# Kernel tuning notes

Hardware: AMD Instinct MI355X
Metric: run time of the kernel (lower is better)

## Reference

```python
import jax, jax.numpy as jnp
import numpy as np

D_MODEL, D_STATE, D_CONV, D_INNER, DT_RANK, K = 96, 16, 3, 192, 6, 4
B, H, W = 1, 64, 64


def setup_inputs() -> dict:
    key = jax.random.key(0)
    ks = jax.random.split(key, 10)
    x = jax.random.normal(ks[0], (B, H, W, D_MODEL), jnp.float32)
    in_proj_w = jax.random.normal(ks[1], (2 * D_INNER, D_MODEL), jnp.float32) * 0.02
    conv_w = jax.random.normal(ks[2], (D_INNER, 1, D_CONV, D_CONV), jnp.float32) * 0.1
    conv_b = jnp.zeros((D_INNER,), jnp.float32)
    x_proj_w = jax.random.normal(ks[3], (K, DT_RANK + 2 * D_STATE, D_INNER), jnp.float32) * 0.02
    dt_std = DT_RANK ** -0.5
    dt_w = jax.random.uniform(ks[4], (K, D_INNER, DT_RANK), jnp.float32, -dt_std, dt_std)
    # dt bias init: inv-softplus of dt ~ logUniform(1e-3, 1e-1)
    u = jax.random.uniform(ks[5], (K, D_INNER), jnp.float32)
    dt = jnp.exp(u * (np.log(0.1) - np.log(0.001)) + np.log(0.001)).clip(1e-4)
    dt_b = dt + jnp.log(-jnp.expm1(-dt))
    A_logs = jnp.log(jnp.broadcast_to(jnp.arange(1, D_STATE + 1, dtype=jnp.float32), (K * D_INNER, D_STATE)))
    Ds = jnp.ones((K * D_INNER,), jnp.float32)
    ln_g = jnp.ones((D_INNER,), jnp.float32)
    ln_b = jnp.zeros((D_INNER,), jnp.float32)
    out_proj_w = jax.random.normal(ks[6], (D_MODEL, D_INNER), jnp.float32) * 0.02
    return dict(x=x, in_proj_w=in_proj_w, conv_w=conv_w, conv_b=conv_b, x_proj_w=x_proj_w,
                dt_w=dt_w, dt_b=dt_b, A_logs=A_logs, Ds=Ds, ln_g=ln_g, ln_b=ln_b,
                out_proj_w=out_proj_w)


def _ss2d(x, in_proj_w, conv_w, conv_b, x_proj_w, dt_w, dt_b, A_logs, Ds, ln_g, ln_b, out_proj_w):
    b, h, w, c = x.shape
    L = h * w
    d = conv_w.shape[0]            # d_inner
    n = A_logs.shape[1]            # d_state
    r = dt_w.shape[2]              # dt_rank
    # in_proj + split
    xz = jnp.einsum('bhwc,ec->bhwe', x, in_proj_w)
    xx, z = xz[..., :d], xz[..., d:]
    # depthwise conv (NCHW) + SiLU
    xc = xx.transpose(0, 3, 1, 2)
    pad = (D_CONV - 1) // 2
    xc = jax.lax.conv_general_dilated(xc, conv_w, (1, 1), [(pad, pad), (pad, pad)],
                                      feature_group_count=d) + conv_b[None, :, None, None]
    xc = jax.nn.silu(xc)
    # 4 scan directions: HW, WH, and their reverses
    x_hw = xc.reshape(b, d, L)
    x_wh = xc.transpose(0, 1, 3, 2).reshape(b, d, L)
    xs = jnp.stack([x_hw, x_wh, x_hw[..., ::-1], x_wh[..., ::-1]], axis=1)  # (b,K,d,L)
    x_dbl = jnp.einsum('bkdl,kcd->bkcl', xs, x_proj_w)
    dts, Bs, Cs = x_dbl[:, :, :r], x_dbl[:, :, r:r + n], x_dbl[:, :, r + n:]
    dts = jnp.einsum('bkrl,kdr->bkdl', dts, dt_w)
    delta = jax.nn.softplus(dts + dt_b[None, :, :, None])        # (b,K,d,L)
    A = -jnp.exp(A_logs).reshape(K, d, n)
    # time-major scanned inputs
    dA = jnp.exp(jnp.einsum('bkdl,kdn->lbkdn', delta, A))        # (L,b,K,d,n)
    dBu = jnp.einsum('bkdl,bknl,bkdl->lbkdn', delta, Bs, xs)
    Ct = Cs.transpose(3, 0, 1, 2)                                # (L,b,K,n)
    def step(hst, inp):
        dA_t, dBu_t, C_t = inp
        hst = dA_t * hst + dBu_t
        return hst, jnp.einsum('bkdn,bkn->bkd', hst, C_t)
    h0 = jnp.zeros((b, K, d, n), jnp.float32)
    _, ys = jax.lax.scan(step, h0, (dA, dBu, Ct))                # ys: (L,b,K,d)
    out_y = ys.transpose(1, 2, 3, 0) + xs * Ds.reshape(K, d)[None, :, :, None]
    # recombine directions
    inv = out_y[:, 2:4][..., ::-1]
    y1 = out_y[:, 0]
    y2 = inv[:, 0]
    wh = out_y[:, 1].reshape(b, d, w, h).transpose(0, 1, 3, 2).reshape(b, d, L)
    invwh = inv[:, 1].reshape(b, d, w, h).transpose(0, 1, 3, 2).reshape(b, d, L)
    y = (y1 + y2 + wh + invwh).transpose(0, 2, 1).reshape(b, h, w, d)
    # LayerNorm (eps=1e-5, torch default)
    mu = y.mean(-1, keepdims=True)
    var = ((y - mu) ** 2).mean(-1, keepdims=True)
    y = (y - mu) * jax.lax.rsqrt(var + 1e-5) * ln_g + ln_b
    y = y * jax.nn.silu(z)
    return jnp.einsum('bhwd,cd->bhwc', y, out_proj_w)


def reference(x, in_proj_w, conv_w, conv_b, x_proj_w, dt_w, dt_b, A_logs, Ds, ln_g, ln_b, out_proj_w):
    return _ss2d(x, in_proj_w, conv_w, conv_b, x_proj_w, dt_w, dt_b, A_logs, Ds, ln_g, ln_b, out_proj_w)
```

## Files before the change

kernel.cpp:

```cpp
#include <hip/hip_runtime.h>
#include <hip/hip_bf16.h>

#define LL 4096
#define DM 96
#define DI 192
#define NS 16
#define RK 6
#define RKP 8
#define KD 4
#define CPROJ 38
#define NC (KD*DI*NS)
#define PT 32
#define WS 196
#define OT 16
#define L2E 1.44269504f

__device__ __forceinline__ float b2f(__hip_bfloat16 v){ return __bfloat162float(v); }

__device__ __forceinline__ void detect_bf16(const unsigned short* __restrict__ xh, int tid, int* sflag){
  if (tid < 64){
    unsigned short u = xh[2*tid];
    int e = (u >> 7) & 0xFF;
    int sane = (e >= 107 && e <= 131) ? 1 : 0;
    unsigned long long m = __ballot(sane);
    if (tid == 0) *sflag = (__popcll(m) >= 32) ? 1 : 0;
  }
}

struct P12 { const void* p[12]; };
__global__ void k_convert_all(P12 ptrs, float* __restrict__ dst) {
  const int off[12] = {0,36864,38592,38784,67968,72576,73344,85632,86400,86592,86784,105216};
  __shared__ int sflag;
  detect_bf16((const unsigned short*)ptrs.p[0], threadIdx.x, &sflag);
  __syncthreads();
  int f = sflag;
  int i = blockIdx.x * 256 + threadIdx.x;
  if (i >= 105216) return;
  int j = 0;
  #pragma unroll
  for (int s = 1; s < 11; s++) if (i >= off[s]) j = s;
  int e = i - off[j];
  const void* src = ptrs.p[j+1];
  if (f) dst[i] = b2f(((const __hip_bfloat16*)src)[e]);
  else   dst[i] = ((const float*)src)[e];
}

__global__ void k_inproj(const void* __restrict__ xraw,
                         const float* __restrict__ w,
                         float* __restrict__ xx, float* __restrict__ z) {
  __shared__ float xr[8*DM];
  __shared__ int sflag;
  int tid = threadIdx.x;
  detect_bf16((const unsigned short*)xraw, tid, &sflag);
  __syncthreads();
  int l0 = blockIdx.x * 8;
  if (sflag){
    const __hip_bfloat16* xb = (const __hip_bfloat16*)xraw + (size_t)l0*DM;
    for (int i = tid; i < 8*DM; i += 384) xr[i] = b2f(xb[i]);
  } else {
    const float* xf = (const float*)xraw + (size_t)l0*DM;
    for (int i = tid; i < 8*DM; i += 384) xr[i] = xf[i];
  }
  __syncthreads();
  int e = tid;
  float acc[8];
  #pragma unroll
  for (int i=0;i<8;i++) acc[i]=0.f;
  const float4* wr4 = (const float4*)(w + (size_t)e*DM);
  #pragma unroll 4
  for (int c4=0;c4<DM/4;c4++){
    float4 wv = wr4[c4];
    int c = c4*4;
    #pragma unroll
    for (int i=0;i<8;i++){
      float a = acc[i];
      a = fmaf(wv.x, xr[i*DM+c  ], a);
      a = fmaf(wv.y, xr[i*DM+c+1], a);
      a = fmaf(wv.z, xr[i*DM+c+2], a);
      a = fmaf(wv.w, xr[i*DM+c+3], a);
      acc[i] = a;
    }
  }
  if (e < DI) {
    #pragma unroll
    for (int i=0;i<8;i++) xx[(l0+i)*DI + e] = acc[i];
  } else {
    int e2 = e - DI;
    #pragma unroll
    for (int i=0;i<8;i++) z[(l0+i)*DI + e2] = acc[i];
  }
}

__global__ void k_conv(const float* __restrict__ xx,
                       const float* __restrict__ cw,
                       const float* __restrict__ cb,
                       float* __restrict__ xc,
                       float* __restrict__ xct) {
  int l = blockIdx.x;
  int d = threadIdx.x;
  int h = l >> 6, w = l & 63;
  float acc = cb[d];
  #pragma unroll
  for (int ki=0; ki<3; ki++){
    int hh = h + ki - 1;
    if ((unsigned)hh >= 64u) continue;
    #pragma unroll
    for (int kj=0;kj<3;kj++){
      int wj = w + kj - 1;
      if ((unsigned)wj >= 64u) continue;
      acc = fmaf(cw[d*9 + ki*3 + kj], xx[(hh*64+wj)*DI + d], acc);
    }
  }
  float v = acc / (1.f + __expf(-acc));
  xc[l*DI + d] = v;
  xct[(((w<<6)|h))*DI + d] = v;
}

__device__ __forceinline__ int dir_map(int k, int t){
  if (k==0) return t;
  if (k==1) return ((t&63)<<6) | (t>>6);
  if (k==2) return 4095 - t;
  int u = 4095 - t; return ((u&63)<<6) | (u>>6);
}

__global__ void __launch_bounds__(256) k_proj(const float* __restrict__ xc,
                       const float* __restrict__ xpw,
                       float* __restrict__ dts,
                       float* __restrict__ Bb, float* __restrict__ Cb) {
  __shared__ float wl[CPROJ*WS];
  __shared__ float xs[PT*WS];
  int b = blockIdx.x;
  int k = b >> 7;
  int t_base = (b & 127) * PT;
  int tid = threadIdx.x;
  for (int idx = tid; idx < CPROJ*DI; idx += 256){
    int cc = idx / DI, j = idx - cc*DI;
    wl[cc*WS + j] = xpw[(k*CPROJ + cc)*DI + j];
  }
  for (int idx = tid; idx < PT*DI; idx += 256){
    int tt = idx / DI, j = idx - tt*DI;
    xs[tt*WS + j] = xc[dir_map(k, t_base + tt)*DI + j];
  }
  __syncthreads();
  int tg = tid & 7;
  int ty = tid >> 3;
  int cc0 = ty;
  int has2 = (ty + 32 < CPROJ);
  int cc1 = has2 ? (ty + 32) : ty;
  float a0x=0.f,a0y=0.f,a0z=0.f,a0w=0.f;
  float a1x=0.f,a1y=0.f,a1z=0.f,a1w=0.f;
  const float4* w0p = (const float4*)&wl[cc0*WS];
  const float4* w1p = (const float4*)&wl[cc1*WS];
  const float4* x0p = (const float4*)&xs[(tg     )*WS];
  const float4* x1p = (const float4*)&xs[(tg +  8)*WS];
  const float4* x2p = (const float4*)&xs[(tg + 16)*WS];
  const float4* x3p = (const float4*)&xs[(tg + 24)*WS];
  #pragma unroll 4
  for (int jc = 0; jc < DI/4; jc++){
    float4 w0 = w0p[jc], w1 = w1p[jc];
    float4 x0 = x0p[jc], x1 = x1p[jc], x2 = x2p[jc], x3 = x3p[jc];
    a0x = fmaf(w0.x,x0.x,fmaf(w0.y,x0.y,fmaf(w0.z,x0.z,fmaf(w0.w,x0.w,a0x))));
    a0y = fmaf(w0.x,x1.x,fmaf(w0.y,x1.y,fmaf(w0.z,x1.z,fmaf(w0.w,x1.w,a0y))));
    a0z = fmaf(w0.x,x2.x,fmaf(w0.y,x2.y,fmaf(w0.z,x2.z,fmaf(w0.w,x2.w,a0z))));
    a0w = fmaf(w0.x,x3.x,fmaf(w0.y,x3.y,fmaf(w0.z,x3.z,fmaf(w0.w,x3.w,a0w))));
    a1x = fmaf(w1.x,x0.x,fmaf(w1.y,x0.y,fmaf(w1.z,x0.z,fmaf(w1.w,x0.w,a1x))));
    a1y = fmaf(w1.x,x1.x,fmaf(w1.y,x1.y,fmaf(w1.z,x1.z,fmaf(w1.w,x1.w,a1y))));
    a1z = fmaf(w1.x,x2.x,fmaf(w1.y,x2.y,fmaf(w1.z,x2.z,fmaf(w1.w,x2.w,a1z))));
    a1w = fmaf(w1.x,x3.x,fmaf(w1.y,x3.y,fmaf(w1.z,x3.z,fmaf(w1.w,x3.w,a1w))));
  }
  float accs0[4] = {a0x,a0y,a0z,a0w};
  float accs1[4] = {a1x,a1y,a1z,a1w};
  #pragma unroll
  for (int i=0;i<4;i++){
    int t = t_base + tg + 8*i;
    size_t kt = (size_t)k*LL + t;
    {
      int cc = cc0; float v = accs0[i];
      if (cc < RK)            dts[kt*RKP + cc] = v;
      else if (cc < RK+NS)    Bb [kt*NS + (cc-RK)] = v;
      else                    Cb [kt*NS + (cc-RK-NS)] = v;
    }
    if (has2){
      int cc = ty + 32; float v = accs1[i];
      if (cc < RK+NS)         Bb [kt*NS + (cc-RK)] = v;
      else                    Cb [kt*NS + (cc-RK-NS)] = v;
    }
  }
}

template<int CHB>
__global__ void __launch_bounds__(192) k_scanA(
                      const float* __restrict__ xc_hw,
                      const float* __restrict__ xc_wh,
                      const float* __restrict__ dts,
                      const float* __restrict__ Bbuf,
                      const float* __restrict__ A_logs,
                      const float* __restrict__ dtw,
                      const float* __restrict__ dtb,
                      float2* __restrict__ PH) {
  constexpr int CS = LL >> CHB;
  __shared__ float ds_[CS*RKP];
  __shared__ float Bs[CS*NS];
  int b = blockIdx.x;
  int k = b >> CHB;
  int c = b & ((1<<CHB)-1);
  int t0 = c*CS;
  int d = threadIdx.x;
  int kd = k*DI + d;
  for (int i = d; i < CS*RKP; i += 192) ds_[i] = dts[((size_t)k*LL + t0)*RKP + i];
  for (int i = d; i < CS*NS;  i += 192) Bs[i]  = Bbuf[((size_t)k*LL + t0)*NS + i];
  float bt = dtb[kd];
  float w0 = dtw[kd*RK+0], w1 = dtw[kd*RK+1], w2 = dtw[kd*RK+2];
  float w3 = dtw[kd*RK+3], w4 = dtw[kd*RK+4], w5 = dtw[kd*RK+5];
  float A2[16], h[16];
  {
    const float4* ap = (const float4*)&A_logs[kd*NS];
    #pragma unroll
    for (int i=0;i<4;i++){
      float4 av = ap[i];
      A2[4*i+0] = -__expf(av.x)*L2E; A2[4*i+1] = -__expf(av.y)*L2E;
      A2[4*i+2] = -__expf(av.z)*L2E; A2[4*i+3] = -__expf(av.w)*L2E;
    }
  }
  #pragma unroll
  for (int n=0;n<16;n++) h[n] = 0.f;
  __syncthreads();
  const float* xbase = (k & 1) ? xc_wh : xc_hw;
  int l0 = (k < 2) ? t0 : (LL-1 - t0);
  int lstep = (k < 2) ? DI : -DI;
  const float* xp = xbase + (size_t)l0*DI + d;
  float cumD = 0.f;
  #pragma unroll 2
  for (int s=0; s<CS; s++){
    float4 lo = *(const float4*)(ds_ + s*RKP);
    float4 hi = *(const float4*)(ds_ + s*RKP + 4);
    float v = bt;
    v = fmaf(w0, lo.x, v); v = fmaf(w1, lo.y, v); v = fmaf(w2, lo.z, v);
    v = fmaf(w3, lo.w, v); v = fmaf(w4, hi.x, v); v = fmaf(w5, hi.y, v);
    float sp = (v > 20.f) ? v : __logf(1.f + __expf(v));
    cumD += sp;
    float sx = sp * xp[(ptrdiff_t)s*lstep];
    #pragma unroll
    for (int n=0;n<16;n++){
      float a = exp2f(sp*A2[n]);
      h[n] = fmaf(a, h[n], sx*Bs[s*NS+n]);
    }
  }
  float2* php = PH + (size_t)c*NC + (size_t)kd*NS;
  #pragma unroll
  for (int n=0;n<16;n++) php[n] = make_float2(exp2f(A2[n]*cumD), h[n]);
}

template<int CHB>
__global__ void __launch_bounds__(256) k_scan2(float2* __restrict__ PH) {
  constexpr int CH = 1 << CHB;
  int idx = blockIdx.x*256 + threadIdx.x;
  float h = 0.f;
  #pragma unroll 8
  for (int c=0;c<CH;c++){
    float2 ph = PH[(size_t)c*NC + idx];
    PH[(size_t)c*NC + idx].y = h;
    h = fmaf(ph.x, h, ph.y);
  }
}

template<int CHB>
__global__ void __launch_bounds__(192) k_scanB(
                      const float* __restrict__ xc_hw,
                      const float* __restrict__ xc_wh,
                      const float* __restrict__ dts,
                      const float* __restrict__ Bbuf,
                      const float* __restrict__ Cbuf,
                      const float* __restrict__ A_logs,
                      const float* __restrict__ dtw,
                      const float* __restrict__ dtb,
                      const float2* __restrict__ PH,
                      float* __restrict__ ydir) {
  constexpr int CS = LL >> CHB;
  __shared__ float ds_[CS*RKP];
  __shared__ float Bs[CS*NS];
  __shared__ float Cs[CS*NS];
  int b = blockIdx.x;
  int k = b >> CHB;
  int c = b & ((1<<CHB)-1);
  int t0 = c*CS;
  int d = threadIdx.x;
  int kd = k*DI + d;
  for (int i = d; i < CS*RKP; i += 192) ds_[i] = dts[((size_t)k*LL + t0)*RKP + i];
  for (int i = d; i < CS*NS;  i += 192) Bs[i]  = Bbuf[((size_t)k*LL + t0)*NS + i];
  for (int i = d; i < CS*NS;  i += 192) Cs[i]  = Cbuf[((size_t)k*LL + t0)*NS + i];
  float bt = dtb[kd];
  float w0 = dtw[kd*RK+0], w1 = dtw[kd*RK+1], w2 = dtw[kd*RK+2];
  float w3 = dtw[kd*RK+3], w4 = dtw[kd*RK+4], w5 = dtw[kd*RK+5];
  float A2[16], h[16];
  {
    const float4* ap = (const float4*)&A_logs[kd*NS];
    #pragma unroll
    for (int i=0;i<4;i++){
      float4 av = ap[i];
      A2[4*i+0] = -__expf(av.x)*L2E; A2[4*i+1] = -__expf(av.y)*L2E;
      A2[4*i+2] = -__expf(av.z)*L2E; A2[4*i+3] = -__expf(av.w)*L2E;
    }
  }
  {
    const float2* hp = PH + (size_t)c*NC + (size_t)kd*NS;
    #pragma unroll
    for (int n=0;n<16;n++) h[n] = hp[n].y;
  }
  __syncthreads();
  const float* xbase = (k & 1) ? xc_wh : xc_hw;
  int l0 = (k < 2) ? t0 : (LL-1 - t0);
  int lstep = (k < 2) ? DI : -DI;
  const float* xp = xbase + (size_t)l0*DI + d;
  float* yp = ydir + ((size_t)k*LL + t0)*DI + d;
  #pragma unroll 2
  for (int s=0; s<CS; s++){
    float4 lo = *(const float4*)(ds_ + s*RKP);
    float4 hi = *(const float4*)(ds_ + s*RKP + 4);
    float v = bt;
    v = fmaf(w0, lo.x, v); v = fmaf(w1, lo.y, v); v = fmaf(w2, lo.z, v);
    v = fmaf(w3, lo.w, v); v = fmaf(w4, hi.x, v); v = fmaf(w5, hi.y, v);
    float sp = (v > 20.f) ? v : __logf(1.f + __expf(v));
    float sx = sp * xp[(ptrdiff_t)s*lstep];
    #pragma unroll
    for (int n=0;n<16;n++){
      float a = exp2f(sp*A2[n]);
      h[n] = fmaf(a, h[n], sx*Bs[s*NS+n]);
    }
    float y0=0.f, y1=0.f, y2=0.f, y3=0.f;
    #pragma unroll
    for (int n=0;n<4;n++){
      y0 = fmaf(h[4*n+0], Cs[s*NS+4*n+0], y0);
      y1 = fmaf(h[4*n+1], Cs[s*NS+4*n+1], y1);
      y2 = fmaf(h[4*n+2], Cs[s*NS+4*n+2], y2);
      y3 = fmaf(h[4*n+3], Cs[s*NS+4*n+3], y3);
    }
    yp[s*DI] = (y0+y1)+(y2+y3);
  }
}

__global__ void __launch_bounds__(192) k_out(
                      const float* __restrict__ ydir,
                      const float* __restrict__ xc,
                      const float* __restrict__ z,
                      const float* __restrict__ Ds,
                      const float* __restrict__ ln_g,
                      const float* __restrict__ ln_b,
                      const float* __restrict__ opw,
                      void* __restrict__ out,
                      const unsigned short* __restrict__ xh) {
  __shared__ float gs[OT*WS];
  __shared__ float ps[2][OT][12];
  __shared__ float mv[2][OT];
  __shared__ int sflag;
  int tid = threadIdx.x;
  int d = tid;
  detect_bf16(xh, tid, &sflag);
  int l0 = blockIdx.x * OT;
  float dsum = Ds[d] + Ds[DI+d] + Ds[2*DI+d] + Ds[3*DI+d];
  #pragma unroll 4
  for (int r=0;r<OT;r++){
    int l = l0 + r;
    int lt = ((l & 63) << 6) | (l >> 6);
    float y = ydir[(size_t)l*DI + d]
            + ydir[((size_t)LL   + lt)*DI + d]
            + ydir[((size_t)2*LL + (4095 - l))*DI + d]
            + ydir[((size_t)3*LL + (4095 - lt))*DI + d];
    gs[r*WS + d] = fmaf(xc[(size_t)l*DI + d], dsum, y);
  }
  __syncthreads();
  {
    int r = tid / 12, lane = tid - r*12;
    float s1 = 0.f, s2 = 0.f;
    for (int j = lane; j < DI; j += 12){
      float v = gs[r*WS + j];
      s1 += v; s2 += v*v;
    }
    ps[0][r][lane] = s1; ps[1][r][lane] = s2;
  }
  __syncthreads();
  if (tid < OT){
    float a = 0.f, bb = 0.f;
    #pragma unroll
    for (int j=0;j<12;j++){ a += ps[0][tid][j]; bb += ps[1][tid][j]; }
    float mu = a * (1.f/192.f);
    float var = bb * (1.f/192.f) - mu*mu;
    mv[0][tid] = mu; mv[1][tid] = rsqrtf(var + 1e-5f);
  }
  __syncthreads();
  float lg = ln_g[d], lb = ln_b[d];
  #pragma unroll 4
  for (int r=0;r<OT;r++){
    float yn = (gs[r*WS + d] - mv[0][r]) * mv[1][r] * lg + lb;
    float zv = z[(size_t)(l0+r)*DI + d];
    gs[r*WS + d] = yn * (zv / (1.f + __expf(-zv)));
  }
  __syncthreads();
  int half = tid / 96;
  int e = tid - half*96;
  int r0 = half*8;
  float acc[8];
  #pragma unroll
  for (int i=0;i<8;i++) acc[i] = 0.f;
  const float4* wrow = (const float4*)(opw + e*DI);
  #pragma unroll 4
  for (int jc = 0; jc < DI/4; jc++){
    float4 w = wrow[jc];
    #pragma unroll
    for (int i=0;i<8;i++){
      float4 gv = *(const float4*)&gs[(r0+i)*WS + jc*4];
      acc[i] = fmaf(w.x,gv.x,fmaf(w.y,gv.y,fmaf(w.z,gv.z,fmaf(w.w,gv.w,acc[i]))));
    }
  }
  int f = sflag;
  #pragma unroll
  for (int i=0;i<8;i++){
    int l = l0 + r0 + i;
    if (f) ((__hip_bfloat16*)out)[l*DM + e] = __float2bfloat16(acc[i]);
    else   ((float*)out)[l*DM + e] = acc[i];
  }
}

extern "C" void kernel_launch(void* const* d_in, const int* in_sizes, int n_in,
                              void* d_out, int out_size, void* d_ws, size_t ws_size,
                              hipStream_t stream) {
  float* ws = (float*)d_ws;
  float* cvt = ws + 16;
  const int off[12] = {0,36864,38592,38784,67968,72576,73344,85632,86400,86592,86784,105216};
  float* c[12];
  c[0] = nullptr;
  for (int i = 1; i < 12; i++) c[i] = cvt + off[i-1];

  float* big    = cvt + 105216;
  float* xx     = big;
  float* z      = xx + (size_t)LL*DI;
  float* xc     = z  + (size_t)LL*DI;
  float* xct    = xc + (size_t)LL*DI;
  float* dts    = xct + (size_t)LL*DI;
  float* Bb     = dts + (size_t)KD*LL*RKP;
  float* Cb     = Bb + (size_t)KD*LL*NS;
  float* PH     = Cb + (size_t)KD*LL*NS;
  size_t need128 = (size_t)(16 + 105216 + 4*786432 + 131072 + 2*262144
                            + 2*128*NC + (size_t)KD*LL*DI) * 4;
  int chBits = (ws_size >= need128) ? 7 : 6;
  int CHn = 1 << chBits;
  float* ydir = PH + 2*(size_t)CHn*NC;

  P12 ptrs;
  for (int i = 0; i < 12; i++) ptrs.p[i] = d_in[i];
  k_convert_all<<<(105216 + 255)/256, 256, 0, stream>>>(ptrs, cvt);

  k_inproj<<<LL/8, 384, 0, stream>>>(d_in[0], c[1], xx, z);
  k_conv<<<LL, DI, 0, stream>>>(xx, c[2], c[3], xc, xct);
  k_proj<<<KD*(LL/PT), 256, 0, stream>>>(xc, c[4], dts, Bb, Cb);
  if (chBits == 7){
    k_scanA<7><<<KD*128, 192, 0, stream>>>(xc, xct, dts, Bb, c[7], c[5], c[6],
                                           (float2*)PH);
    k_scan2<7><<<NC/256, 256, 0, stream>>>((float2*)PH);
    k_scanB<7><<<KD*128, 192, 0, stream>>>(xc, xct, dts, Bb, Cb, c[7], c[5], c[6],
                                           (const float2*)PH, ydir);
  } else {
    k_scanA<6><<<KD*64, 192, 0, stream>>>(xc, xct, dts, Bb, c[7], c[5], c[6],
                                          (float2*)PH);
    k_scan2<6><<<NC/256, 256, 0, stream>>>((float2*)PH);
    k_scanB<6><<<KD*64, 192, 0, stream>>>(xc, xct, dts, Bb, Cb, c[7], c[5], c[6],
                                          (const float2*)PH, ydir);
  }
  k_out<<<LL/OT, 192, 0, stream>>>(ydir, xc, z, c[8], c[9], c[10], c[11], d_out,
                                   (const unsigned short*)d_in[0]);
}
```

Before: 206.3 us.

## Fuse conversion into in_proj, drop transposed copy, scatter scan outputs, finer chunks

Merges the weight-conversion kernel into the in_proj kernel, and in_proj now reads its weight directly from the raw input, so one launch is removed. The transposed xc copy is dropped: the scan kernels index xc through dir_map and write ydir in spatial order, which makes k_out's gather contiguous. The chunk carry now stores cumD per channel plus h, not a per-state decay and h pair, and the decay is recomputed in k_scan2. The chunk count rises to 256 when the workspace allows, and k_out tiles shrink to 8 rows. The row-indexed xc reads and ydir writes in the scans become strided for the transposed directions, and the longer k_scan2 serial loop may offset the gains.

```diff
diff --git a/kernel.cpp b/kernel.cpp
--- a/kernel.cpp
+++ b/kernel.cpp
@@ -9,12 +9,17 @@
 #define RKP 8
 #define KD 4
 #define CPROJ 38
+#define NCH (KD*DI)
 #define NC (KD*DI*NS)
 #define PT 32
 #define WS 196
-#define OT 16
+#define OT 8
 #define L2E 1.44269504f
 
+__device__ __forceinline__ float bf2f(unsigned short u){
+  unsigned int x = ((unsigned int)u) << 16;
+  return __uint_as_float(x);
+}
 __device__ __forceinline__ float b2f(__hip_bfloat16 v){ return __bfloat162float(v); }
 
 __device__ __forceinline__ void detect_bf16(const unsigned short* __restrict__ xh, int tid, int* sflag){
@@ -27,100 +32,105 @@
   }
 }
 
-struct P12 { const void* p[12]; };
-__global__ void k_convert_all(P12 ptrs, float* __restrict__ dst) {
-  const int off[12] = {0,36864,38592,38784,67968,72576,73344,85632,86400,86592,86784,105216};
-  __shared__ int sflag;
-  detect_bf16((const unsigned short*)ptrs.p[0], threadIdx.x, &sflag);
-  __syncthreads();
-  int f = sflag;
-  int i = blockIdx.x * 256 + threadIdx.x;
-  if (i >= 105216) return;
-  int j = 0;
-  #pragma unroll
-  for (int s = 1; s < 11; s++) if (i >= off[s]) j = s;
-  int e = i - off[j];
-  const void* src = ptrs.p[j+1];
-  if (f) dst[i] = b2f(((const __hip_bfloat16*)src)[e]);
-  else   dst[i] = ((const float*)src)[e];
-}
-
-__global__ void k_inproj(const void* __restrict__ xraw,
-                         const float* __restrict__ w,
-                         float* __restrict__ xx, float* __restrict__ z) {
-  __shared__ float xr[8*DM];
-  __shared__ int sflag;
-  int tid = threadIdx.x;
-  detect_bf16((const unsigned short*)xraw, tid, &sflag);
-  __syncthreads();
-  int l0 = blockIdx.x * 8;
-  if (sflag){
-    const __hip_bfloat16* xb = (const __hip_bfloat16*)xraw + (size_t)l0*DM;
-    for (int i = tid; i < 8*DM; i += 384) xr[i] = b2f(xb[i]);
-  } else {
-    const float* xf = (const float*)xraw + (size_t)l0*DM;
-    for (int i = tid; i < 8*DM; i += 384) xr[i] = xf[i];
-  }
-  __syncthreads();
-  int e = tid;
-  float acc[8];
-  #pragma unroll
-  for (int i=0;i<8;i++) acc[i]=0.f;
-  const float4* wr4 = (const float4*)(w + (size_t)e*DM);
-  #pragma unroll 4
-  for (int c4=0;c4<DM/4;c4++){
-    float4 wv = wr4[c4];
-    int c = c4*4;
-    #pragma unroll
-    for (int i=0;i<8;i++){
-      float a = acc[i];
-      a = fmaf(wv.x, xr[i*DM+c  ], a);
-      a = fmaf(wv.y, xr[i*DM+c+1], a);
-      a = fmaf(wv.z, xr[i*DM+c+2], a);
-      a = fmaf(wv.w, xr[i*DM+c+3], a);
-      acc[i] = a;
-    }
-  }
-  if (e < DI) {
-    #pragma unroll
-    for (int i=0;i<8;i++) xx[(l0+i)*DI + e] = acc[i];
-  } else {
-    int e2 = e - DI;
-    #pragma unroll
-    for (int i=0;i<8;i++) z[(l0+i)*DI + e2] = acc[i];
-  }
-}
-
-__global__ void k_conv(const float* __restrict__ xx,
-                       const float* __restrict__ cw,
-                       const float* __restrict__ cb,
-                       float* __restrict__ xc,
-                       float* __restrict__ xct) {
-  int l = blockIdx.x;
-  int d = threadIdx.x;
-  int h = l >> 6, w = l & 63;
-  float acc = cb[d];
-  #pragma unroll
-  for (int ki=0; ki<3; ki++){
-    int hh = h + ki - 1;
-    if ((unsigned)hh >= 64u) continue;
-    #pragma unroll
-    for (int kj=0;kj<3;kj++){
-      int wj = w + kj - 1;
-      if ((unsigned)wj >= 64u) continue;
-      acc = fmaf(cw[d*9 + ki*3 + kj], xx[(hh*64+wj)*DI + d], acc);
-    }
-  }
-  float v = acc / (1.f + __expf(-acc));
-  xc[l*DI + d] = v;
-  xct[(((w<<6)|h))*DI + d] = v;
-}
-
 __device__ __forceinline__ int dir_map(int k, int t){
   if (k==0) return t;
   if (k==1) return ((t&63)<<6) | (t>>6);
   if (k==2) return 4095 - t;
   int u = 4095 - t; return ((u&63)<<6) | (u>>6);
+}
+
+struct P12 { const void* p[12]; };
+
+__global__ void __launch_bounds__(384) k_inprojcvt(P12 ptrs, float* __restrict__ cvt,
+                         float* __restrict__ xx, float* __restrict__ z) {
+  __shared__ float xr[8*DM];
+  __shared__ int sflag;
+  int tid = threadIdx.x;
+  detect_bf16((const unsigned short*)ptrs.p[0], tid, &sflag);
+  __syncthreads();
+  int f = sflag;
+  if (blockIdx.x >= LL/8){
+    const int off[12] = {0,36864,38592,38784,67968,72576,73344,85632,86400,86592,86784,105216};
+    int i = (blockIdx.x - LL/8)*384 + tid + 36864;
+    if (i < 105216){
+      int j = 1;
+      #pragma unroll
+      for (int s = 2; s < 11; s++) if (i >= off[s]) j = s;
+      int e = i - off[j];
+      const void* src = ptrs.p[j+1];
+      cvt[i] = f ? b2f(((const __hip_bfloat16*)src)[e]) : ((const float*)src)[e];
+    }
+    return;
+  }
+  int l0 = blockIdx.x * 8;
+  if (f){
+    const __hip_bfloat16* xb = (const __hip_bfloat16*)ptrs.p[0] + (size_t)l0*DM;
+    for (int i = tid; i < 8*DM; i += 384) xr[i] = b2f(xb[i]);
+  } else {
+    const float* xf = (const float*)ptrs.p[0] + (size_t)l0*DM;
+    for (int i = tid; i < 8*DM; i += 384) xr[i] = xf[i];
+  }
+  __syncthreads();
+  int e = tid;
+  float acc[8];
+  #pragma unroll
+  for (int i=0;i<8;i++) acc[i]=0.f;
+  const float4* xr4 = (const float4*)xr;
+  if (f){
+    const ushort4* wb = (const ushort4*)((const unsigned short*)ptrs.p[1] + (size_t)e*DM);
+    #pragma unroll 4
+    for (int c4=0;c4<DM/4;c4++){
+      ushort4 uv = wb[c4];
+      float4 wv = make_float4(bf2f(uv.x), bf2f(uv.y), bf2f(uv.z), bf2f(uv.w));
+      #pragma unroll
+      for (int i=0;i<8;i++){
+        float4 xv = xr4[i*24 + c4];
+        acc[i] = fmaf(wv.x,xv.x,fmaf(wv.y,xv.y,fmaf(wv.z,xv.z,fmaf(wv.w,xv.w,acc[i]))));
+      }
+    }
+  } else {
+    const float4* wr4 = (const float4*)((const float*)ptrs.p[1] + (size_t)e*DM);
+    #pragma unroll 4
+    for (int c4=0;c4<DM/4;c4++){
+      float4 wv = wr4[c4];
+      #pragma unroll
+      for (int i=0;i<8;i++){
+        float4 xv = xr4[i*24 + c4];
+        acc[i] = fmaf(wv.x,xv.x,fmaf(wv.y,xv.y,fmaf(wv.z,xv.z,fmaf(wv.w,xv.w,acc[i]))));
+      }
+    }
+  }
+  if (e < DI) {
+    #pragma unroll
+    for (int i=0;i<8;i++) xx[(l0+i)*DI + e] = acc[i];
+  } else {
+    int e2 = e - DI;
+    #pragma unroll
+    for (int i=0;i<8;i++) z[(l0+i)*DI + e2] = acc[i];
+  }
+}
+
+__global__ void k_conv(const float* __restrict__ xx,
+                       const float* __restrict__ cw,
+                       const float* __restrict__ cb,
+                       float* __restrict__ xc) {
+  int l = blockIdx.x;
+  int d = threadIdx.x;
+  int h = l >> 6, w = l & 63;
+  float acc = cb[d];
+  #pragma unroll
+  for (int ki=0; ki<3; ki++){
+    int hh = h + ki - 1;
+    if ((unsigned)hh >= 64u) continue;
+    #pragma unroll
+    for (int kj=0;kj<3;kj++){
+      int wj = w + kj - 1;
+      if ((unsigned)wj >= 64u) continue;
+      acc = fmaf(cw[d*9 + ki*3 + kj], xx[(hh*64+wj)*DI + d], acc);
+    }
+  }
+  float v = acc / (1.f + __expf(-acc));
+  xc[l*DI + d] = v;
 }
 
 __global__ void __launch_bounds__(256) k_proj(const float* __restrict__ xc,
@@ -190,14 +200,14 @@
 
 template<int CHB>
 __global__ void __launch_bounds__(192) k_scanA(
-                      const float* __restrict__ xc_hw,
-                      const float* __restrict__ xc_wh,
+                      const float* __restrict__ xc,
                       const float* __restrict__ dts,
                       const float* __restrict__ Bbuf,
                       const float* __restrict__ A_logs,
                       const float* __restrict__ dtw,
                       const float* __restrict__ dtb,
-                      float2* __restrict__ PH) {
+                      float* __restrict__ cumDbuf,
+                      float* __restrict__ Harr) {
   constexpr int CS = LL >> CHB;
   __shared__ float ds_[CS*RKP];
   __shared__ float Bs[CS*NS];
@@ -225,10 +235,6 @@
   #pragma unroll
   for (int n=0;n<16;n++) h[n] = 0.f;
   __syncthreads();
-  const float* xbase = (k & 1) ? xc_wh : xc_hw;
-  int l0 = (k < 2) ? t0 : (LL-1 - t0);
-  int lstep = (k < 2) ? DI : -DI;
-  const float* xp = xbase + (size_t)l0*DI + d;
   float cumD = 0.f;
   #pragma unroll 2
   for (int s=0; s<CS; s++){
@@ -239,42 +245,56 @@
     v = fmaf(w3, lo.w, v); v = fmaf(w4, hi.x, v); v = fmaf(w5, hi.y, v);
     float sp = (v > 20.f) ? v : __logf(1.f + __expf(v));
     cumD += sp;
-    float sx = sp * xp[(ptrdiff_t)s*lstep];
+    int row = dir_map(k, t0 + s);
+    float sx = sp * xc[(size_t)row*DI + d];
+    float4 b0 = *(const float4*)(Bs + s*NS);
+    float4 b1 = *(const float4*)(Bs + s*NS + 4);
+    float4 b2 = *(const float4*)(Bs + s*NS + 8);
+    float4 b3 = *(const float4*)(Bs + s*NS + 12);
+    float bb[16] = {b0.x,b0.y,b0.z,b0.w, b1.x,b1.y,b1.z,b1.w,
+                    b2.x,b2.y,b2.z,b2.w, b3.x,b3.y,b3.z,b3.w};
     #pragma unroll
     for (int n=0;n<16;n++){
       float a = exp2f(sp*A2[n]);
-      h[n] = fmaf(a, h[n], sx*Bs[s*NS+n]);
-    }
-  }
-  float2* php = PH + (size_t)c*NC + (size_t)kd*NS;
-  #pragma unroll
-  for (int n=0;n<16;n++) php[n] = make_float2(exp2f(A2[n]*cumD), h[n]);
+      h[n] = fmaf(a, h[n], sx*bb[n]);
+    }
+  }
+  cumDbuf[(size_t)c*NCH + kd] = cumD;
+  float4* hp = (float4*)(Harr + ((size_t)c*NCH + kd)*16);
+  hp[0] = make_float4(h[0],h[1],h[2],h[3]);
+  hp[1] = make_float4(h[4],h[5],h[6],h[7]);
+  hp[2] = make_float4(h[8],h[9],h[10],h[11]);
+  hp[3] = make_float4(h[12],h[13],h[14],h[15]);
 }
 
 template<int CHB>
-__global__ void __launch_bounds__(256) k_scan2(float2* __restrict__ PH) {
+__global__ void __launch_bounds__(256) k_scan2(const float* __restrict__ A_logs,
+                                               const float* __restrict__ cumDbuf,
+                                               float* __restrict__ Harr) {
   constexpr int CH = 1 << CHB;
   int idx = blockIdx.x*256 + threadIdx.x;
+  int kd = idx >> 4;
+  float A2 = -__expf(A_logs[idx]) * L2E;
   float h = 0.f;
-  #pragma unroll 8
+  #pragma unroll 4
   for (int c=0;c<CH;c++){
-    float2 ph = PH[(size_t)c*NC + idx];
-    PH[(size_t)c*NC + idx].y = h;
-    h = fmaf(ph.x, h, ph.y);
+    float hl = Harr[(size_t)c*NC + idx];
+    float P = exp2f(A2 * cumDbuf[(size_t)c*NCH + kd]);
+    Harr[(size_t)c*NC + idx] = h;
+    h = fmaf(P, h, hl);
   }
 }
 
 template<int CHB>
 __global__ void __launch_bounds__(192) k_scanB(
-                      const float* __restrict__ xc_hw,
-                      const float* __restrict__ xc_wh,
+                      const float* __restrict__ xc,
                       const float* __restrict__ dts,
                       const float* __restrict__ Bbuf,
                       const float* __restrict__ Cbuf,
                       const float* __restrict__ A_logs,
                       const float* __restrict__ dtw,
                       const float* __restrict__ dtb,
-                      const float2* __restrict__ PH,
+                      const float* __restrict__ Harr,
                       float* __restrict__ ydir) {
   constexpr int CS = LL >> CHB;
   __shared__ float ds_[CS*RKP];
@@ -303,16 +323,14 @@
     }
   }
   {
-    const float2* hp = PH + (size_t)c*NC + (size_t)kd*NS;
-    #pragma unroll
-    for (int n=0;n<16;n++) h[n] = hp[n].y;
-  }
-  __syncthreads();
-  const float* xbase = (k & 1) ? xc_wh : xc_hw;
-  int l0 = (k < 2) ? t0 : (LL-1 - t0);
-  int lstep = (k < 2) ? DI : -DI;
-  const float* xp = xbase + (size_t)l0*DI + d;
-  float* yp = ydir + ((size_t)k*LL + t0)*DI + d;
+    const float4* hp = (const float4*)(Harr + ((size_t)c*NCH + kd)*16);
+    float4 h0 = hp[0], h1 = hp[1], h2 = hp[2], h3 = hp[3];
+    h[0]=h0.x; h[1]=h0.y; h[2]=h0.z; h[3]=h0.w;
+    h[4]=h1.x; h[5]=h1.y; h[6]=h1.z; h[7]=h1.w;
+    h[8]=h2.x; h[9]=h2.y; h[10]=h2.z; h[11]=h2.w;
+    h[12]=h3.x; h[13]=h3.y; h[14]=h3.z; h[15]=h3.w;
+  }
+  __syncthreads();
   #pragma unroll 2
   for (int s=0; s<CS; s++){
     float4 lo = *(const float4*)(ds_ + s*RKP);
@@ -321,21 +339,34 @@
     v = fmaf(w0, lo.x, v); v = fmaf(w1, lo.y, v); v = fmaf(w2, lo.z, v);
     v = fmaf(w3, lo.w, v); v = fmaf(w4, hi.x, v); v = fmaf(w5, hi.y, v);
     float sp = (v > 20.f) ? v : __logf(1.f + __expf(v));
-    float sx = sp * xp[(ptrdiff_t)s*lstep];
+    int row = dir_map(k, t0 + s);
+    float sx = sp * xc[(size_t)row*DI + d];
+    float4 b0 = *(const float4*)(Bs + s*NS);
+    float4 b1 = *(const float4*)(Bs + s*NS + 4);
+    float4 b2 = *(const float4*)(Bs + s*NS + 8);
+    float4 b3 = *(const float4*)(Bs + s*NS + 12);
+    float bb[16] = {b0.x,b0.y,b0.z,b0.w, b1.x,b1.y,b1.z,b1.w,
+                    b2.x,b2.y,b2.z,b2.w, b3.x,b3.y,b3.z,b3.w};
     #pragma unroll
     for (int n=0;n<16;n++){
       float a = exp2f(sp*A2[n]);
-      h[n] = fmaf(a, h[n], sx*Bs[s*NS+n]);
-    }
+      h[n] = fmaf(a, h[n], sx*bb[n]);
+    }
+    float4 c0 = *(const float4*)(Cs + s*NS);
+    float4 c1 = *(const float4*)(Cs + s*NS + 4);
+    float4 c2 = *(const float4*)(Cs + s*NS + 8);
+    float4 c3 = *(const float4*)(Cs + s*NS + 12);
+    float cc[16] = {c0.x,c0.y,c0.z,c0.w, c1.x,c1.y,c1.z,c1.w,
+                    c2.x,c2.y,c2.z,c2.w, c3.x,c3.y,c3.z,c3.w};
     float y0=0.f, y1=0.f, y2=0.f, y3=0.f;
     #pragma unroll
     for (int n=0;n<4;n++){
-      y0 = fmaf(h[4*n+0], Cs[s*NS+4*n+0], y0);
-      y1 = fmaf(h[4*n+1], Cs[s*NS+4*n+1], y1);
-      y2 = fmaf(h[4*n+2], Cs[s*NS+4*n+2], y2);
-      y3 = fmaf(h[4*n+3], Cs[s*NS+4*n+3], y3);
-    }
-    yp[s*DI] = (y0+y1)+(y2+y3);
+      y0 = fmaf(h[4*n+0], cc[4*n+0], y0);
+      y1 = fmaf(h[4*n+1], cc[4*n+1], y1);
+      y2 = fmaf(h[4*n+2], cc[4*n+2], y2);
+      y3 = fmaf(h[4*n+3], cc[4*n+3], y3);
+    }
+    ydir[((size_t)k*LL + row)*DI + d] = (y0+y1)+(y2+y3);
   }
 }
 
@@ -350,7 +381,7 @@
                       void* __restrict__ out,
                       const unsigned short* __restrict__ xh) {
   __shared__ float gs[OT*WS];
-  __shared__ float ps[2][OT][12];
+  __shared__ float ps[2][OT][24];
   __shared__ float mv[2][OT];
   __shared__ int sflag;
   int tid = threadIdx.x;
@@ -358,21 +389,21 @@
   detect_bf16(xh, tid, &sflag);
   int l0 = blockIdx.x * OT;
   float dsum = Ds[d] + Ds[DI+d] + Ds[2*DI+d] + Ds[3*DI+d];
-  #pragma unroll 4
+  #pragma unroll
   for (int r=0;r<OT;r++){
-    int l = l0 + r;
-    int lt = ((l & 63) << 6) | (l >> 6);
-    float y = ydir[(size_t)l*DI + d]
-            + ydir[((size_t)LL   + lt)*DI + d]
-            + ydir[((size_t)2*LL + (4095 - l))*DI + d]
-            + ydir[((size_t)3*LL + (4095 - lt))*DI + d];
-    gs[r*WS + d] = fmaf(xc[(size_t)l*DI + d], dsum, y);
+    size_t ld = (size_t)(l0+r)*DI + d;
+    float y = ydir[ld]
+            + ydir[(size_t)LL*DI   + ld]
+            + ydir[(size_t)2*LL*DI + ld]
+            + ydir[(size_t)3*LL*DI + ld];
+    gs[r*WS + d] = fmaf(xc[ld], dsum, y);
   }
   __syncthreads();
   {
-    int r = tid / 12, lane = tid - r*12;
+    int r = tid / 24, lane = tid - r*24;
     float s1 = 0.f, s2 = 0.f;
-    for (int j = lane; j < DI; j += 12){
+    #pragma unroll
+    for (int j = lane; j < DI; j += 24){
       float v = gs[r*WS + j];
       s1 += v; s2 += v*v;
     }
@@ -382,14 +413,14 @@
   if (tid < OT){
     float a = 0.f, bb = 0.f;
     #pragma unroll
-    for (int j=0;j<12;j++){ a += ps[0][tid][j]; bb += ps[1][tid][j]; }
+    for (int j=0;j<24;j++){ a += ps[0][tid][j]; bb += ps[1][tid][j]; }
     float mu = a * (1.f/192.f);
     float var = bb * (1.f/192.f) - mu*mu;
     mv[0][tid] = mu; mv[1][tid] = rsqrtf(var + 1e-5f);
   }
   __syncthreads();
   float lg = ln_g[d], lb = ln_b[d];
-  #pragma unroll 4
+  #pragma unroll
   for (int r=0;r<OT;r++){
     float yn = (gs[r*WS + d] - mv[0][r]) * mv[1][r] * lg + lb;
     float zv = z[(size_t)(l0+r)*DI + d];
@@ -398,23 +429,23 @@
   __syncthreads();
   int half = tid / 96;
   int e = tid - half*96;
-  int r0 = half*8;
-  float acc[8];
-  #pragma unroll
-  for (int i=0;i<8;i++) acc[i] = 0.f;
+  int r0 = half*4;
+  float acc[4];
+  #pragma unroll
+  for (int i=0;i<4;i++) acc[i] = 0.f;
   const float4* wrow = (const float4*)(opw + e*DI);
   #pragma unroll 4
   for (int jc = 0; jc < DI/4; jc++){
     float4 w = wrow[jc];
     #pragma unroll
-    for (int i=0;i<8;i++){
+    for (int i=0;i<4;i++){
       float4 gv = *(const float4*)&gs[(r0+i)*WS + jc*4];
       acc[i] = fmaf(w.x,gv.x,fmaf(w.y,gv.y,fmaf(w.z,gv.z,fmaf(w.w,gv.w,acc[i]))));
     }
   }
   int f = sflag;
   #pragma unroll
-  for (int i=0;i<8;i++){
+  for (int i=0;i<4;i++){
     int l = l0 + r0 + i;
     if (f) ((__hip_bfloat16*)out)[l*DM + e] = __float2bfloat16(acc[i]);
     else   ((float*)out)[l*DM + e] = acc[i];
@@ -431,40 +462,36 @@
   c[0] = nullptr;
   for (int i = 1; i < 12; i++) c[i] = cvt + off[i-1];
 
-  float* big    = cvt + 105216;
-  float* xx     = big;
-  float* z      = xx + (size_t)LL*DI;
-  float* xc     = z  + (size_t)LL*DI;
-  float* xct    = xc + (size_t)LL*DI;
-  float* dts    = xct + (size_t)LL*DI;
-  float* Bb     = dts + (size_t)KD*LL*RKP;
-  float* Cb     = Bb + (size_t)KD*LL*NS;
-  float* PH     = Cb + (size_t)KD*LL*NS;
-  size_t need128 = (size_t)(16 + 105216 + 4*786432 + 131072 + 2*262144
-                            + 2*128*NC + (size_t)KD*LL*DI) * 4;
-  int chBits = (ws_size >= need128) ? 7 : 6;
+  float* xx   = cvt + 105216;
+  float* z    = xx + (size_t)LL*DI;
+  float* xc   = z  + (size_t)LL*DI;
+  float* dts  = xc + (size_t)LL*DI;
+  float* Bb   = dts + (size_t)KD*LL*RKP;
+  float* Cb   = Bb + (size_t)KD*LL*NS;
+  float* cumD = Cb + (size_t)KD*LL*NS;
+
+  size_t fixed = 16 + 105216 + 3*(size_t)LL*DI + (size_t)KD*LL*RKP
+               + 2*(size_t)KD*LL*NS + (size_t)KD*LL*DI;
+  size_t need8 = (fixed + 256*(size_t)(NCH + NC)) * 4;
+  int chBits = (ws_size >= need8) ? 8 : 6;
   int CHn = 1 << chBits;
-  float* ydir = PH + 2*(size_t)CHn*NC;
+  float* Harr = cumD + (size_t)CHn*NCH;
+  float* ydir = Harr + (size_t)CHn*NC;
 
   P12 ptrs;
   for (int i = 0; i < 12; i++) ptrs.p[i] = d_in[i];
-  k_convert_all<<<(105216 + 255)/256, 256, 0, stream>>>(ptrs, cvt);
-
-  k_inproj<<<LL/8, 384, 0, stream>>>(d_in[0], c[1], xx, z);
-  k_conv<<<LL, DI, 0, stream>>>(xx, c[2], c[3], xc, xct);
+
+  k_inprojcvt<<<LL/8 + 178, 384, 0, stream>>>(ptrs, cvt, xx, z);
+  k_conv<<<LL, DI, 0, stream>>>(xx, c[2], c[3], xc);
   k_proj<<<KD*(LL/PT), 256, 0, stream>>>(xc, c[4], dts, Bb, Cb);
-  if (chBits == 7){
-    k_scanA<7><<<KD*128, 192, 0, stream>>>(xc, xct, dts, Bb, c[7], c[5], c[6],
-                                           (float2*)PH);
-    k_scan2<7><<<NC/256, 256, 0, stream>>>((float2*)PH);
-    k_scanB<7><<<KD*128, 192, 0, stream>>>(xc, xct, dts, Bb, Cb, c[7], c[5], c[6],
-                                           (const float2*)PH, ydir);
+  if (chBits == 8){
+    k_scanA<8><<<KD*256, 192, 0, stream>>>(xc, dts, Bb, c[7], c[5], c[6], cumD, Harr);
+    k_scan2<8><<<NC/256, 256, 0, stream>>>(c[7], cumD, Harr);
+    k_scanB<8><<<KD*256, 192, 0, stream>>>(xc, dts, Bb, Cb, c[7], c[5], c[6], Harr, ydir);
   } else {
-    k_scanA<6><<<KD*64, 192, 0, stream>>>(xc, xct, dts, Bb, c[7], c[5], c[6],
-                                          (float2*)PH);
-    k_scan2<6><<<NC/256, 256, 0, stream>>>((float2*)PH);
-    k_scanB<6><<<KD*64, 192, 0, stream>>>(xc, xct, dts, Bb, Cb, c[7], c[5], c[6],
-                                          (const float2*)PH, ydir);
+    k_scanA<6><<<KD*64, 192, 0, stream>>>(xc, dts, Bb, c[7], c[5], c[6], cumD, Harr);
+    k_scan2<6><<<NC/256, 256, 0, stream>>>(c[7], cumD, Harr);
+    k_scanB<6><<<KD*64, 192, 0, stream>>>(xc, dts, Bb, Cb, c[7], c[5], c[6], Harr, ydir);
   }
   k_out<<<LL/OT, 192, 0, stream>>>(ydir, xc, z, c[8], c[9], c[10], c[11], d_out,
                                    (const unsigned short*)d_in[0]);
```

After: 220.1 us. 1.07x slower.
